# Kernel tuning notes

Measured on AMD Instinct MI355X. Metric: run time of the kernel, lower is better.

## Reference

```python
import jax, jax.numpy as jnp
import numpy as np

N_NODES = 50000      # nodes
N_EDGES = 800000     # edges (avg degree 16)
D = 128              # input_dim == hidden_dim
C = 32               # output_dim (classes)
G = 64               # number of graphs in batch
EPS = 1e-5           # LayerNorm eps (torch default)
NUM_LAYERS = 3


def setup_inputs() -> dict:
    key = jax.random.key(0)
    ks = jax.random.split(key, 12)
    scale = 1.0 / np.sqrt(D)
    x = jax.random.normal(ks[0], (N_NODES, D), dtype=jnp.float32)
    edge_index = jax.random.randint(ks[1], (2, N_EDGES), 0, N_NODES)
    batch = jnp.sort(jax.random.randint(ks[2], (N_NODES,), 0, G))
    # CustomConv params: self-loop linear + message linear, 3 layers stacked
    W_self = jax.random.normal(ks[3], (NUM_LAYERS, D, D), dtype=jnp.float32) * scale
    b_self = jnp.zeros((NUM_LAYERS, D), dtype=jnp.float32)
    W_msg = jax.random.normal(ks[4], (NUM_LAYERS, D, D), dtype=jnp.float32) * scale
    b_msg = jnp.zeros((NUM_LAYERS, D), dtype=jnp.float32)
    # two LayerNorms (after layers 0 and 1)
    ln_g = jnp.ones((2, D), dtype=jnp.float32)
    ln_b = jnp.zeros((2, D), dtype=jnp.float32)
    # post-MP MLP head: Linear(D,D) -> Dropout(identity in eval) -> Linear(D,C)
    W1 = jax.random.normal(ks[5], (D, D), dtype=jnp.float32) * scale
    b1 = jnp.zeros((D,), dtype=jnp.float32)
    W2 = jax.random.normal(ks[6], (D, C), dtype=jnp.float32) * scale
    b2 = jnp.zeros((C,), dtype=jnp.float32)
    return {"x": x, "W_self": W_self, "b_self": b_self, "W_msg": W_msg,
            "b_msg": b_msg, "ln_g": ln_g, "ln_b": ln_b, "W1": W1, "b1": b1,
            "W2": W2, "b2": b2, "edge_index": edge_index, "batch": batch}


def _layer_norm(h, g, b):
    mu = jnp.mean(h, axis=-1, keepdims=True)
    var = jnp.mean(jnp.square(h - mu), axis=-1, keepdims=True)
    return g * (h - mu) * jax.lax.rsqrt(var + EPS) + b


def reference(x, W_self, b_self, W_msg, b_msg, ln_g, ln_b, W1, b1, W2, b2,
              edge_index, batch):
    src, dst = edge_index[0], edge_index[1]
    for i in range(NUM_LAYERS):
        # CustomConv: self linear + sum-aggregated neighbor messages
        msg = x @ W_msg[i] + b_msg[i]                     # [N, D]
        agg = jax.ops.segment_sum(msg[src], dst, num_segments=N_NODES)
        x = x @ W_self[i] + b_self[i] + agg               # [N, D]
        x = jax.nn.relu(x)
        # dropout p=0.25 is identity in eval mode
        if i != NUM_LAYERS - 1:
            x = _layer_norm(x, ln_g[i], ln_b[i])
    # global mean pool over graphs
    sums = jax.ops.segment_sum(x, batch, num_segments=G)          # [G, D]
    cnt = jax.ops.segment_sum(jnp.ones((N_NODES,), x.dtype), batch,
                              num_segments=G)                     # [G]
    pooled = sums / jnp.maximum(cnt, 1.0)[:, None]
    # post-MP head (dropout identity in eval)
    h = pooled @ W1 + b1
    logits = h @ W2 + b2                                          # [G, C]
    return jax.nn.log_softmax(logits, axis=1)
```

## Files before the change

kernel.cpp:

```cpp
#include <hip/hip_runtime.h>
#include <hip/hip_bf16.h>
#include <math.h>

#define N_NODES 50000
#define N_EDGES 800000
#define DIM 128
#define CLS 32
#define NGRAPH 64
#define LN_EPS 1e-5f
#define NBLK 196
#define ABLK 256
#define EPB (N_EDGES / ABLK)
#define EB_STRIDE 7168
#define LCAP 8192
#define ROWS1 (N_NODES + 1)

typedef __attribute__((ext_vector_type(8))) short bf16x8;
typedef __attribute__((ext_vector_type(4))) float f32x4;

static __device__ __forceinline__ int lower_bound_i(const int* a, int n, int key) {
    int lo = 0, hi = n;
    while (lo < hi) { int mid = (lo + hi) >> 1; if (a[mid] < key) lo = mid + 1; else hi = mid; }
    return lo;
}

static __device__ __forceinline__ void acc8(float* ac, uint4 v) {
    unsigned int u[4] = {v.x, v.y, v.z, v.w};
#pragma unroll
    for (int k = 0; k < 4; k++) {
        union { unsigned int b; float f; } lo, hi;
        lo.b = u[k] << 16;
        hi.b = u[k] & 0xffff0000u;
        ac[2 * k] += lo.f;
        ac[2 * k + 1] += hi.f;
    }
}

static __device__ __forceinline__ void drain_node(const __hip_bfloat16* __restrict__ Xb,
                                                  const unsigned short* __restrict__ csr,
                                                  int b, int e, int seg, int cl, float* ac) {
    for (; b + 16 <= e; b += 16) {
        int idx16 = csr[b + cl];
        int s[4];
        uint4 v[4];
#pragma unroll
        for (int r = 0; r < 4; r++) s[r] = __shfl(idx16, r * 4 + seg, 64);
#pragma unroll
        for (int r = 0; r < 4; r++) v[r] = *(const uint4*)(Xb + (size_t)s[r] * DIM + cl * 8);
#pragma unroll
        for (int r = 0; r < 4; r++) acc8(ac, v[r]);
    }
    if (b < e) {
        int idx8 = csr[b + (cl & 7)];
        int s0 = __shfl(idx8, seg, 64);
        int s1 = __shfl(idx8, 4 + seg, 64);
        uint4 v0 = *(const uint4*)(Xb + (size_t)s0 * DIM + cl * 8);
        uint4 v1 = *(const uint4*)(Xb + (size_t)s1 * DIM + cl * 8);
        acc8(ac, v0);
        acc8(ac, v1);
    }
}


__global__ __launch_bounds__(256) void prep_kernel(
    const float* __restrict__ x, const float* __restrict__ Wself,
    const float* __restrict__ Wmsg, __hip_bfloat16* __restrict__ XbIn,
    __hip_bfloat16* __restrict__ WT,
    int* __restrict__ ecur, float* __restrict__ gsum,
    __hip_bfloat16* __restrict__ padA, __hip_bfloat16* __restrict__ padB,
    __hip_bfloat16* __restrict__ padC) {
    int i = blockIdx.x * 256 + threadIdx.x;
    if (i < N_NODES * DIM / 2) {
        float2 v = ((const float2*)x)[i];
        ((__hip_bfloat162*)XbIn)[i] = __float22bfloat162_rn(v);
    }
    if (i < 3 * 128 * 256) {
        int l = i / (128 * 256);
        int rem = i - l * (128 * 256);
        int n = rem >> 8;
        int k = rem & 255;
        float v = (k < 128) ? Wself[l * 16384 + k * 128 + n]
                            : Wmsg[l * 16384 + (k - 128) * 128 + n];
        WT[i] = __float2bfloat16(v);
    }
    if (i < NBLK) ecur[i] = i * EB_STRIDE;
    if (i < NGRAPH * DIM) gsum[i] = 0.f;
    if (i < DIM) {
        padA[i] = __float2bfloat16(0.f);
        padB[i] = __float2bfloat16(0.f);
        padC[i] = __float2bfloat16(0.f);
    }
}


__global__ __launch_bounds__(1024) void bucket_kernel(
    const int* __restrict__ esrc, const int* __restrict__ edst,
    int* __restrict__ ecur, int* __restrict__ ebuf) {
    __shared__ int bc4[4][NBLK];
    __shared__ int bc[NBLK], bres[NBLK], bcnt[NBLK];
    const int t = threadIdx.x;
    const int e0 = blockIdx.x * EPB;
    for (int i = t; i < 4 * NBLK; i += 1024) ((int*)bc4)[i] = 0;
    __syncthreads();
    int dr[4], sr[4];
#pragma unroll
    for (int it = 0; it < 4; it++) {
        int i = t + it * 1024;
        if (i < EPB) { dr[it] = edst[e0 + i]; sr[it] = esrc[e0 + i]; }
        else { dr[it] = -1; sr[it] = 0; }
    }
    const int cpy = (t >> 6) & 3;
#pragma unroll
    for (int it = 0; it < 4; it++)
        if (dr[it] >= 0) atomicAdd(&bc4[cpy][dr[it] >> 8], 1);
    __syncthreads();
    if (t < NBLK) {
        int c = bc4[0][t] + bc4[1][t] + bc4[2][t] + bc4[3][t];
        int r = (c + 7) & ~7;
        int res = atomicAdd(&ecur[t], r);
        bres[t] = res;
        bcnt[t] = c;
        bc[t] = res;
    }
    __syncthreads();
#pragma unroll
    for (int it = 0; it < 4; it++)
        if (dr[it] >= 0) {
            int d = dr[it];
            int pos = atomicAdd(&bc[d >> 8], 1);
            ebuf[pos] = ((d & 255) << 16) | sr[it];
        }
    __syncthreads();
    if (t < NBLK) {
        int c = bcnt[t], r = (c + 7) & ~7, base = bres[t];
        for (int j = c; j < r; j++) ebuf[base + j] = -1;
    }
}


__global__ __launch_bounds__(1024) void csr_fused_kernel(
    const int* __restrict__ ebuf, const int* __restrict__ ecur,
    int* __restrict__ counts, int* __restrict__ off,
    unsigned short* __restrict__ csr) {
    __shared__ int ncnt[256];
    __shared__ int ssc[256];
    __shared__ int cur[256];
    __shared__ unsigned short lcsr[LCAP];
    const int b = blockIdx.x, t = threadIdx.x;
    const int used = ecur[b] - b * EB_STRIDE;
    const int* eb = ebuf + b * EB_STRIDE;
    for (int i = t; i < LCAP / 2; i += 1024)
        ((unsigned int*)lcsr)[i] = 0xC350C350u;
    if (t < 256) ncnt[t] = 0;
    __syncthreads();
    for (int i = t; i < used; i += 1024) {
        int p = eb[i];
        if (p != -1) atomicAdd(&ncnt[p >> 16], 1);
    }
    __syncthreads();
    int myc = 0, mypad = 0;
    const int gi = b * 256 + t;
    if (t < 256) {
        myc = (gi < N_NODES) ? ncnt[t] : 0;
        mypad = (myc + 7) & ~7;
        ssc[t] = mypad;
    }
    __syncthreads();
    for (int o = 1; o < 256; o <<= 1) {
        int v = 0;
        if (t < 256 && t >= o) v = ssc[t - o];
        __syncthreads();
        if (t < 256) ssc[t] += v;
        __syncthreads();
    }
    if (t < 256) {
        int eoff = ssc[t] - mypad;
        cur[t] = eoff;
        if (gi < N_NODES) {
            off[gi] = b * LCAP + eoff;
            counts[gi] = myc;
        }
    }
    __syncthreads();
    for (int i = t; i < used; i += 1024) {
        int p = eb[i];
        if (p != -1) {
            int pos = atomicAdd(&cur[p >> 16], 1);
            lcsr[pos] = (unsigned short)(p & 0xFFFF);
        }
    }
    __syncthreads();
    const int total = ssc[255];
    int4* dst4 = (int4*)(csr + (size_t)b * LCAP);
    const int4* src4 = (const int4*)lcsr;
    for (int i = t; i < (total >> 3); i += 1024) dst4[i] = src4[i];
}


__global__ __launch_bounds__(256) void layer_fused_kernel(
    const __hip_bfloat16* __restrict__ Xb,
    const int* __restrict__ off, const int* __restrict__ counts,
    const unsigned short* __restrict__ csr,
    const __hip_bfloat16* __restrict__ WT,
    const float* __restrict__ bself, const float* __restrict__ bmsg,
    const float* __restrict__ lng, const float* __restrict__ lnb,
    const int* __restrict__ batch, float* __restrict__ gsum,
    __hip_bfloat16* __restrict__ XoutB, int do_ln, int do_pool) {
    __shared__ __hip_bfloat16 wlds[128 * 136];
    __shared__ __hip_bfloat16 slds[64 * 136];
    const int tid = threadIdx.x;
    const int w = tid >> 6, lane = tid & 63;
    const int l15 = lane & 15, q = lane >> 4;
    const int rowblk = blockIdx.x * 64;
    const int growbase = rowblk + w * 16;

    {
        int n = tid >> 1, h = tid & 1;
        const uint4* src = (const uint4*)(WT + n * 256 + h * 64);
        uint4* dst = (uint4*)(&wlds[n * 136 + h * 64]);
#pragma unroll
        for (int i = 0; i < 8; i++) dst[i] = src[i];
    }

    const int seg = lane >> 4, cl = lane & 15;
    for (int j = 0; j < 16; j += 2) {
        int na = growbase + j;
        int nb = na + 1;
        int ba = 0, ea = 0, bb = 0, eb2 = 0;
        if (na < N_NODES) { ba = off[na]; ea = ba + ((counts[na] + 7) & ~7); }
        if (nb < N_NODES) { bb = off[nb]; eb2 = bb + ((counts[nb] + 7) & ~7); }
        float aa[8], ab[8];
#pragma unroll
        for (int k = 0; k < 8; k++) { aa[k] = 0.f; ab[k] = 0.f; }
        while (ba + 16 <= ea && bb + 16 <= eb2) {
            int ia = csr[ba + cl];
            int ib = csr[bb + cl];
            int sa[4], sb[4];
#pragma unroll
            for (int r = 0; r < 4; r++) {
                sa[r] = __shfl(ia, r * 4 + seg, 64);
                sb[r] = __shfl(ib, r * 4 + seg, 64);
            }
            uint4 va[4], vb[4];
#pragma unroll
            for (int r = 0; r < 4; r++) va[r] = *(const uint4*)(Xb + (size_t)sa[r] * DIM + cl * 8);
#pragma unroll
            for (int r = 0; r < 4; r++) vb[r] = *(const uint4*)(Xb + (size_t)sb[r] * DIM + cl * 8);
#pragma unroll
            for (int r = 0; r < 4; r++) acc8(aa, va[r]);
#pragma unroll
            for (int r = 0; r < 4; r++) acc8(ab, vb[r]);
            ba += 16;
            bb += 16;
        }
        drain_node(Xb, csr, ba, ea, seg, cl, aa);
        drain_node(Xb, csr, bb, eb2, seg, cl, ab);
#pragma unroll
        for (int k = 0; k < 8; k++) {
            aa[k] += __shfl_xor(aa[k], 16, 64);
            aa[k] += __shfl_xor(aa[k], 32, 64);
            ab[k] += __shfl_xor(ab[k], 16, 64);
            ab[k] += __shfl_xor(ab[k], 32, 64);
        }
        if (lane < 16) {
            union { uint4 u; __hip_bfloat162 h[4]; } pa, pb;
#pragma unroll
            for (int k = 0; k < 4; k++) {
                pa.h[k] = __float22bfloat162_rn(make_float2(aa[2 * k], aa[2 * k + 1]));
                pb.h[k] = __float22bfloat162_rn(make_float2(ab[2 * k], ab[2 * k + 1]));
            }
            *(uint4*)(&slds[(w * 16 + j) * 136 + cl * 8]) = pa.u;
            *(uint4*)(&slds[(w * 16 + j + 1) * 136 + cl * 8]) = pb.u;
        }
    }

    f32x4 acc[8];
#pragma unroll
    for (int ct = 0; ct < 8; ct++) acc[ct] = (f32x4){0.f, 0.f, 0.f, 0.f};

    __syncthreads();

    const int row = growbase + l15;
    const int rowc = min(row, N_NODES);
    const __hip_bfloat16* arow = Xb + (size_t)rowc * DIM;
#pragma unroll
    for (int ks = 0; ks < 4; ks++) {
        bf16x8 afrag = *(const bf16x8*)(arow + ks * 32 + q * 8);
#pragma unroll
        for (int ct = 0; ct < 8; ct++) {
            bf16x8 bfrag = *(const bf16x8*)(&wlds[(ct * 16 + l15) * 136 + ks * 32 + q * 8]);
            acc[ct] = __builtin_amdgcn_mfma_f32_16x16x32_bf16(afrag, bfrag, acc[ct], 0, 0, 0);
        }
    }
    __syncthreads();
    {
        int n = tid >> 1, h = tid & 1;
        const uint4* src = (const uint4*)(WT + n * 256 + 128 + h * 64);
        uint4* dst = (uint4*)(&wlds[n * 136 + h * 64]);
#pragma unroll
        for (int i = 0; i < 8; i++) dst[i] = src[i];
    }
    __syncthreads();
#pragma unroll
    for (int ks = 0; ks < 4; ks++) {
        bf16x8 afrag = *(const bf16x8*)(&slds[(w * 16 + l15) * 136 + ks * 32 + q * 8]);
#pragma unroll
        for (int ct = 0; ct < 8; ct++) {
            bf16x8 bfrag = *(const bf16x8*)(&wlds[(ct * 16 + l15) * 136 + ks * 32 + q * 8]);
            acc[ct] = __builtin_amdgcn_mfma_f32_16x16x32_bf16(afrag, bfrag, acc[ct], 0, 0, 0);
        }
    }

    float racc[8];
#pragma unroll
    for (int ct = 0; ct < 8; ct++) racc[ct] = 0.f;
    int gw = 0;
    bool fastp = false;
    if (do_pool) {
        int first = (growbase < N_NODES) ? growbase : (N_NODES - 1);
        gw = batch[first];
        int lastrow = growbase + 15;
        fastp = (growbase < N_NODES) && (lastrow < N_NODES) && (batch[lastrow] == gw);
    }
#pragma unroll
    for (int r = 0; r < 4; r++) {
        int grow = growbase + q * 4 + r;
        bool valid = grow < N_NODES;
        float dg = valid ? (float)counts[grow] : 0.f;
        float v[8];
        float s1 = 0.f;
#pragma unroll
        for (int ct = 0; ct < 8; ct++) {
            int col = ct * 16 + l15;
            float h = acc[ct][r] + bself[col] + dg * bmsg[col];
            h = fmaxf(h, 0.f);
            v[ct] = h;
            s1 += h;
        }
        if (do_ln) {
#pragma unroll
            for (int m = 1; m < 16; m <<= 1) s1 += __shfl_xor(s1, m, 64);
            float mu = s1 * (1.0f / 128.0f);
            float s2 = 0.f;
#pragma unroll
            for (int ct = 0; ct < 8; ct++) { float d = v[ct] - mu; s2 += d * d; }
#pragma unroll
            for (int m = 1; m < 16; m <<= 1) s2 += __shfl_xor(s2, m, 64);
            float rs = rsqrtf(s2 * (1.0f / 128.0f) + LN_EPS);
#pragma unroll
            for (int ct = 0; ct < 8; ct++) {
                int col = ct * 16 + l15;
                v[ct] = lng[col] * (v[ct] - mu) * rs + lnb[col];
            }
        }
        if (do_pool) {
            if (fastp) {
#pragma unroll
                for (int ct = 0; ct < 8; ct++) racc[ct] += v[ct];
            } else if (valid) {
                int g = batch[grow];
#pragma unroll
                for (int ct = 0; ct < 8; ct++)
                    atomicAdd(&gsum[g * DIM + ct * 16 + l15], v[ct]);
            }
        } else if (valid) {
#pragma unroll
            for (int ct = 0; ct < 8; ct++) {
                int col = ct * 16 + l15;
                XoutB[(size_t)grow * DIM + col] = __float2bfloat16(v[ct]);
            }
        }
    }
    if (do_pool && fastp) {
#pragma unroll
        for (int ct = 0; ct < 8; ct++) {
            racc[ct] += __shfl_xor(racc[ct], 16, 64);
            racc[ct] += __shfl_xor(racc[ct], 32, 64);
        }
        if (q == 0) {
#pragma unroll
            for (int ct = 0; ct < 8; ct++)
                atomicAdd(&gsum[gw * DIM + ct * 16 + l15], racc[ct]);
        }
    }
}


__global__ __launch_bounds__(128) void head_kernel(
    const float* __restrict__ gsum, const int* __restrict__ batch,
    const float* __restrict__ W1, const float* __restrict__ b1,
    const float* __restrict__ W2, const float* __restrict__ b2,
    float* __restrict__ out) {
    __shared__ float p[128];
    __shared__ float hh[128];
    int g = blockIdx.x;
    int j = threadIdx.x;
    int lo = lower_bound_i(batch, N_NODES, g);
    int hi = lower_bound_i(batch, N_NODES, g + 1);
    float cnt = fmaxf((float)(hi - lo), 1.0f);
    p[j] = gsum[g * DIM + j] / cnt;
    __syncthreads();
    float s = b1[j];
    for (int k = 0; k < DIM; k++) s += p[k] * W1[k * DIM + j];
    hh[j] = s;
    __syncthreads();
    if (j < CLS) {
        float l = b2[j];
        for (int k = 0; k < DIM; k++) l += hh[k] * W2[k * CLS + j];
        float mx = l;
#pragma unroll
        for (int m = 16; m >= 1; m >>= 1) mx = fmaxf(mx, __shfl_xor(mx, m, 64));
        float ex = expf(l - mx);
        float se = ex;
#pragma unroll
        for (int m = 16; m >= 1; m >>= 1) se += __shfl_xor(se, m, 64);
        out[g * CLS + j] = l - mx - logf(se);
    }
}


extern "C" void kernel_launch(void* const* d_in, const int* in_sizes, int n_in,
                              void* d_out, int out_size, void* d_ws, size_t ws_size,
                              hipStream_t stream) {
    (void)in_sizes; (void)n_in; (void)out_size; (void)ws_size;
    const float* x     = (const float*)d_in[0];
    const float* Wself = (const float*)d_in[1];
    const float* bself = (const float*)d_in[2];
    const float* Wmsg  = (const float*)d_in[3];
    const float* bmsg  = (const float*)d_in[4];
    const float* lng   = (const float*)d_in[5];
    const float* lnb   = (const float*)d_in[6];
    const float* W1    = (const float*)d_in[7];
    const float* b1    = (const float*)d_in[8];
    const float* W2    = (const float*)d_in[9];
    const float* b2    = (const float*)d_in[10];
    const int*   ei    = (const int*)d_in[11];
    const int*   batch = (const int*)d_in[12];
    const int* esrc = ei;
    const int* edst = ei + N_EDGES;

    char* w = (char*)d_ws;
    size_t o = 0;
    auto alloc = [&](size_t bytes) { void* p = w + o; o += (bytes + 255) & ~(size_t)255; return p; };
    __hip_bfloat16* XbIn = (__hip_bfloat16*)alloc((size_t)ROWS1 * DIM * 2);
    __hip_bfloat16* Xb0  = (__hip_bfloat16*)alloc((size_t)ROWS1 * DIM * 2);
    __hip_bfloat16* Xb1  = (__hip_bfloat16*)alloc((size_t)ROWS1 * DIM * 2);
    __hip_bfloat16* WT   = (__hip_bfloat16*)alloc((size_t)3 * 128 * 256 * 2);
    int*   counts = (int*)alloc((size_t)N_NODES * 4);
    int*   offs   = (int*)alloc((size_t)(N_NODES + 1) * 4);
    int*   ecur   = (int*)alloc((size_t)NBLK * 4);
    int*   ebuf   = (int*)alloc((size_t)NBLK * EB_STRIDE * 4);
    unsigned short* csr = (unsigned short*)alloc((size_t)NBLK * LCAP * 2);
    float* gsum   = (float*)alloc((size_t)NGRAPH * DIM * 4);

    prep_kernel<<<(N_NODES * DIM / 2 + 255) / 256, 256, 0, stream>>>(
        x, Wself, Wmsg, XbIn, WT, ecur, gsum,
        XbIn + (size_t)N_NODES * DIM, Xb0 + (size_t)N_NODES * DIM,
        Xb1 + (size_t)N_NODES * DIM);

    bucket_kernel<<<ABLK, 1024, 0, stream>>>(esrc, edst, ecur, ebuf);
    csr_fused_kernel<<<NBLK, 1024, 0, stream>>>(ebuf, ecur, counts, offs, csr);

    const __hip_bfloat16* XbCur = XbIn;
    __hip_bfloat16* bbufs[3] = {Xb0, Xb1, Xb0};
    for (int i = 0; i < 3; i++) {
        layer_fused_kernel<<<(N_NODES + 63) / 64, 256, 0, stream>>>(
            XbCur, offs, counts, csr, WT + (size_t)i * 128 * 256,
            bself + i * DIM, bmsg + i * DIM,
            (i < 2) ? lng + i * DIM : lng, (i < 2) ? lnb + i * DIM : lnb,
            batch, gsum,
            bbufs[i], (i < 2) ? 1 : 0, (i == 2) ? 1 : 0);
        XbCur = bbufs[i];
    }

    head_kernel<<<NGRAPH, 128, 0, stream>>>(gsum, batch, W1, b1, W2, b2, (float*)d_out);
}
```

Baseline: 311.4 us.

## Prepack weights in MFMA fragment order and read B fragments from global

The prep kernel now writes the bf16 weights already permuted into the per-lane MFMA B-fragment layout. The layer kernel then loads each fragment straight from global/L2 with one coalesced 16-byte load per lane, instead of staging the weights into LDS. This drops the 34 KB weight LDS buffer, both staging copies and three block barriers, which should raise occupancy and shorten the prologue. The cost is that every wave re-reads the 64 KB weight block per layer from cache rather than sharing one copy through LDS.

After: 334.2 us. 7.3% more time.

```diff
diff --git a/kernel.cpp b/kernel.cpp
--- a/kernel.cpp
+++ b/kernel.cpp
@@ -65,7 +65,7 @@
 __global__ __launch_bounds__(256) void prep_kernel(
     const float* __restrict__ x, const float* __restrict__ Wself,
     const float* __restrict__ Wmsg, __hip_bfloat16* __restrict__ XbIn,
-    __hip_bfloat16* __restrict__ WT,
+    __hip_bfloat16* __restrict__ WTf,
     int* __restrict__ ecur, float* __restrict__ gsum,
     __hip_bfloat16* __restrict__ padA, __hip_bfloat16* __restrict__ padB,
     __hip_bfloat16* __restrict__ padC) {
@@ -74,14 +74,19 @@
         float2 v = ((const float2*)x)[i];
         ((__hip_bfloat162*)XbIn)[i] = __float22bfloat162_rn(v);
     }
-    if (i < 3 * 128 * 256) {
-        int l = i / (128 * 256);
-        int rem = i - l * (128 * 256);
-        int n = rem >> 8;
-        int k = rem & 255;
+    if (i < 3 * 32768) {
+        int l = i >> 15;
+        int rem = i & 32767;
+        int ct = rem >> 12;
+        int kk = (rem >> 9) & 7;
+        int lane = (rem >> 3) & 63;
+        int e = rem & 7;
+        int q = lane >> 4, l15 = lane & 15;
+        int n = ct * 16 + l15;
+        int k = kk * 32 + q * 8 + e;
         float v = (k < 128) ? Wself[l * 16384 + k * 128 + n]
                             : Wmsg[l * 16384 + (k - 128) * 128 + n];
-        WT[i] = __float2bfloat16(v);
+        WTf[i] = __float2bfloat16(v);
     }
     if (i < NBLK) ecur[i] = i * EB_STRIDE;
     if (i < NGRAPH * DIM) gsum[i] = 0.f;
@@ -201,26 +206,17 @@
     const __hip_bfloat16* __restrict__ Xb,
     const int* __restrict__ off, const int* __restrict__ counts,
     const unsigned short* __restrict__ csr,
-    const __hip_bfloat16* __restrict__ WT,
+    const __hip_bfloat16* __restrict__ WTf,
     const float* __restrict__ bself, const float* __restrict__ bmsg,
     const float* __restrict__ lng, const float* __restrict__ lnb,
     const int* __restrict__ batch, float* __restrict__ gsum,
     __hip_bfloat16* __restrict__ XoutB, int do_ln, int do_pool) {
-    __shared__ __hip_bfloat16 wlds[128 * 136];
     __shared__ __hip_bfloat16 slds[64 * 136];
     const int tid = threadIdx.x;
     const int w = tid >> 6, lane = tid & 63;
     const int l15 = lane & 15, q = lane >> 4;
     const int rowblk = blockIdx.x * 64;
     const int growbase = rowblk + w * 16;
-
-    {
-        int n = tid >> 1, h = tid & 1;
-        const uint4* src = (const uint4*)(WT + n * 256 + h * 64);
-        uint4* dst = (uint4*)(&wlds[n * 136 + h * 64]);
-#pragma unroll
-        for (int i = 0; i < 8; i++) dst[i] = src[i];
-    }
 
     const int seg = lane >> 4, cl = lane & 15;
     for (int j = 0; j < 16; j += 2) {
@@ -278,8 +274,6 @@
 #pragma unroll
     for (int ct = 0; ct < 8; ct++) acc[ct] = (f32x4){0.f, 0.f, 0.f, 0.f};
 
-    __syncthreads();
-
     const int row = growbase + l15;
     const int rowc = min(row, N_NODES);
     const __hip_bfloat16* arow = Xb + (size_t)rowc * DIM;
@@ -288,25 +282,16 @@
         bf16x8 afrag = *(const bf16x8*)(arow + ks * 32 + q * 8);
 #pragma unroll
         for (int ct = 0; ct < 8; ct++) {
-            bf16x8 bfrag = *(const bf16x8*)(&wlds[(ct * 16 + l15) * 136 + ks * 32 + q * 8]);
+            bf16x8 bfrag = *(const bf16x8*)(WTf + (((ct * 8 + ks) * 64) + lane) * 8);
             acc[ct] = __builtin_amdgcn_mfma_f32_16x16x32_bf16(afrag, bfrag, acc[ct], 0, 0, 0);
         }
     }
-    __syncthreads();
-    {
-        int n = tid >> 1, h = tid & 1;
-        const uint4* src = (const uint4*)(WT + n * 256 + 128 + h * 64);
-        uint4* dst = (uint4*)(&wlds[n * 136 + h * 64]);
-#pragma unroll
-        for (int i = 0; i < 8; i++) dst[i] = src[i];
-    }
-    __syncthreads();
 #pragma unroll
     for (int ks = 0; ks < 4; ks++) {
         bf16x8 afrag = *(const bf16x8*)(&slds[(w * 16 + l15) * 136 + ks * 32 + q * 8]);
 #pragma unroll
         for (int ct = 0; ct < 8; ct++) {
-            bf16x8 bfrag = *(const bf16x8*)(&wlds[(ct * 16 + l15) * 136 + ks * 32 + q * 8]);
+            bf16x8 bfrag = *(const bf16x8*)(WTf + (((ct * 8 + 4 + ks) * 64) + lane) * 8);
             acc[ct] = __builtin_amdgcn_mfma_f32_16x16x32_bf16(afrag, bfrag, acc[ct], 0, 0, 0);
         }
     }
@@ -445,7 +430,7 @@
     __hip_bfloat16* XbIn = (__hip_bfloat16*)alloc((size_t)ROWS1 * DIM * 2);
     __hip_bfloat16* Xb0  = (__hip_bfloat16*)alloc((size_t)ROWS1 * DIM * 2);
     __hip_bfloat16* Xb1  = (__hip_bfloat16*)alloc((size_t)ROWS1 * DIM * 2);
-    __hip_bfloat16* WT   = (__hip_bfloat16*)alloc((size_t)3 * 128 * 256 * 2);
+    __hip_bfloat16* WTf  = (__hip_bfloat16*)alloc((size_t)3 * 32768 * 2);
     int*   counts = (int*)alloc((size_t)N_NODES * 4);
     int*   offs   = (int*)alloc((size_t)(N_NODES + 1) * 4);
     int*   ecur   = (int*)alloc((size_t)NBLK * 4);
@@ -454,7 +439,7 @@
     float* gsum   = (float*)alloc((size_t)NGRAPH * DIM * 4);
 
     prep_kernel<<<(N_NODES * DIM / 2 + 255) / 256, 256, 0, stream>>>(
-        x, Wself, Wmsg, XbIn, WT, ecur, gsum,
+        x, Wself, Wmsg, XbIn, WTf, ecur, gsum,
         XbIn + (size_t)N_NODES * DIM, Xb0 + (size_t)N_NODES * DIM,
         Xb1 + (size_t)N_NODES * DIM);
 
@@ -465,7 +450,7 @@
     __hip_bfloat16* bbufs[3] = {Xb0, Xb1, Xb0};
     for (int i = 0; i < 3; i++) {
         layer_fused_kernel<<<(N_NODES + 63) / 64, 256, 0, stream>>>(
-            XbCur, offs, counts, csr, WT + (size_t)i * 128 * 256,
+            XbCur, offs, counts, csr, WTf + (size_t)i * 32768,
             bself + i * DIM, bmsg + i * DIM,
             (i < 2) ? lng + i * DIM : lng, (i < 2) ? lnb + i * DIM : lnb,
             batch, gsum,
```
